# Performance work log

Hardware: AMD Instinct MI355X
Metric: run time of the kernel (lower is better)

Reference implementation:

```python
import jax, jax.numpy as jnp
import numpy as np

B, N, F_IN, OUT = 1, 8192, 256, 64

def setup_inputs() -> dict:
    key = jax.random.key(0)
    k1, k2, k3, k4 = jax.random.split(key, 4)
    seq = jax.random.normal(k1, (B, N, F_IN), dtype=jnp.float32)
    bias_mat = jnp.zeros((B, N, N), dtype=jnp.float32)  # 0 = fully connected; -1e9 entries mask edges
    W1 = jax.random.normal(k2, (F_IN, OUT), dtype=jnp.float32) * 0.05
    a1 = jax.random.normal(k3, (OUT, 1), dtype=jnp.float32) * 0.05
    b1 = jnp.zeros((1,), dtype=jnp.float32)
    a2 = jax.random.normal(k4, (OUT, 1), dtype=jnp.float32) * 0.05
    b2 = jnp.zeros((1,), dtype=jnp.float32)
    return {"seq": seq, "bias_mat": bias_mat, "W1": W1, "a1": a1, "b1": b1, "a2": a2, "b2": b2}

def reference(seq, bias_mat, W1, a1, b1, a2, b2):
    # Conv1D(kernel=1) == matmul over the feature dim
    seq_fts = jnp.einsum('bnf,fo->bno', seq, W1)          # [B,N,OUT]
    f_1 = jnp.einsum('bno,ok->bnk', seq_fts, a1) + b1      # [B,N,1]
    f_2 = jnp.einsum('bno,ok->bnk', seq_fts, a2) + b2      # [B,N,1]
    logits = f_1 + jnp.swapaxes(f_2, 1, 2)                  # [B,N,N] additive outer-sum
    coefs = jax.nn.softmax(jax.nn.leaky_relu(logits, negative_slope=0.2) + bias_mat, axis=-1)
    vals = jnp.einsum('bnm,bmo->bno', coefs, seq_fts)       # [B,N,OUT]
    return jax.nn.elu(vals)
```

## Files before the change

kernel.cpp:

```cpp
#include <hip/hip_runtime.h>
#include <hip/hip_bf16.h>


typedef float f32x4 __attribute__((ext_vector_type(4)));
typedef short bf16x8 __attribute__((ext_vector_type(8)));

__device__ __forceinline__ unsigned short f2bf(float x) {
    union { float f; unsigned u; } v; v.f = x;
    unsigned r = v.u + 0x7FFF + ((v.u >> 16) & 1);
    return (unsigned short)(r >> 16);
}

__device__ __forceinline__ float elu1(float x) {
    return x > 0.f ? x : (__expf(x) - 1.f);
}

__global__ __launch_bounds__(256) void attn_fts(
    const float* __restrict__ seq, const float* __restrict__ W1,
    const float* __restrict__ a1, const float* __restrict__ b1,
    const float* __restrict__ a2, const float* __restrict__ b2,
    unsigned short* __restrict__ ftsT, float* __restrict__ f1g,
    float* __restrict__ f2g)
{
    __shared__ unsigned short w1t[64 * 264];
    __shared__ unsigned short stage[64 * 40];
    __shared__ float f1p[2][32];
    __shared__ float f2p[2][32];

    const int tid = threadIdx.x;
    const int qb = blockIdx.x * 32;
    const int w = tid >> 6, rg = w & 1, oh = w >> 1;
    const int lane = tid & 63, c = lane & 15, g = lane >> 4;

    for (int i = 0; i < 64; ++i) {
        int e = tid + i * 256;
        int k = e >> 6, o = e & 63;
        w1t[o * 264 + k] = f2bf(W1[e]);
    }
    __syncthreads();

    f32x4 acc[2] = {};
    const float* srow = seq + (long)(qb + rg * 16 + c) * 256;
    #pragma unroll
    for (int ks = 0; ks < 8; ++ks) {
        int k0 = ks * 32 + g * 8;
        float4 s0 = *(const float4*)(srow + k0);
        float4 s1 = *(const float4*)(srow + k0 + 4);
        bf16x8 af;
        af[0] = (short)f2bf(s0.x); af[1] = (short)f2bf(s0.y);
        af[2] = (short)f2bf(s0.z); af[3] = (short)f2bf(s0.w);
        af[4] = (short)f2bf(s1.x); af[5] = (short)f2bf(s1.y);
        af[6] = (short)f2bf(s1.z); af[7] = (short)f2bf(s1.w);
        #pragma unroll
        for (int ob = 0; ob < 2; ++ob) {
            int brow = oh * 32 + ob * 16 + c;
            bf16x8 bf = *(const bf16x8*)(&w1t[brow * 264 + k0]);
            acc[ob] = __builtin_amdgcn_mfma_f32_16x16x32_bf16(af, bf, acc[ob], 0, 0, 0);
        }
    }

    float a1v0 = a1[oh * 32 + c], a1v1 = a1[oh * 32 + 16 + c];
    float a2v0 = a2[oh * 32 + c], a2v1 = a2[oh * 32 + 16 + c];
    #pragma unroll
    for (int reg = 0; reg < 4; ++reg) {
        float p1 = acc[0][reg] * a1v0 + acc[1][reg] * a1v1;
        float p2 = acc[0][reg] * a2v0 + acc[1][reg] * a2v1;
        #pragma unroll
        for (int mm = 1; mm < 16; mm <<= 1) {
            p1 += __shfl_xor(p1, mm, 64);
            p2 += __shfl_xor(p2, mm, 64);
        }
        if (c == 0) {
            f1p[oh][rg * 16 + g * 4 + reg] = p1;
            f2p[oh][rg * 16 + g * 4 + reg] = p2;
        }
    }

    #pragma unroll
    for (int ob = 0; ob < 2; ++ob) {
        int row = oh * 32 + ob * 16 + c;
        #pragma unroll
        for (int rp = 0; rp < 2; ++rp) {
            unsigned short lo = f2bf(acc[ob][rp * 2]);
            unsigned short hi = f2bf(acc[ob][rp * 2 + 1]);
            unsigned v = (unsigned)lo | ((unsigned)hi << 16);
            *(unsigned*)(&stage[row * 40 + rg * 16 + g * 4 + rp * 2]) = v;
        }
    }
    __syncthreads();

    {
        int o = tid >> 2, q4 = tid & 3;
        uint4 v = *(const uint4*)(&stage[o * 40 + q4 * 8]);
        *(uint4*)(&ftsT[(long)o * 8192 + qb + q4 * 8]) = v;
    }
    if (tid < 32) {
        f1g[qb + tid] = f1p[0][tid] + f1p[1][tid] + b1[0];
        f2g[qb + tid] = f2p[0][tid] + f2p[1][tid] + b2[0];
    }
}

__global__ __launch_bounds__(512) void attn_main(
    const float* __restrict__ bias, const unsigned short* __restrict__ ftsT,
    const float* __restrict__ f1g, const float* __restrict__ f2g,
    float* __restrict__ out)
{
    __shared__ float bias_lds[2][32][132];
    __shared__ unsigned short fts_lds[2][64][136];
    __shared__ float macc[2][4][16][68];
    __shared__ float mlm[2][4][16];
    __shared__ float mll[2][4][16];

    const int tid = threadIdx.x;
    const int qb = blockIdx.x * 32;
    const int w = tid >> 6, rg = w & 1, h = w >> 1;
    const int lane = tid & 63, c = lane & 15, g = lane >> 4;

    const int srow = tid >> 4;
    const int ssub = tid & 15;
    const long brow_base = (long)(qb + srow) * 8192;
    const int frow = tid >> 3;
    const int fchunk = tid & 7;

    const float f1r = f1g[qb + rg * 16 + c];

    float4 pb0, pb1, pf2a, pf2b;
    uint4 pf0, pf1;
    {
        const float* bp = bias + brow_base + ssub * 8;
        pb0 = ((const float4*)bp)[0];
        pb1 = ((const float4*)bp)[1];
        const unsigned short* fp = ftsT + (long)frow * 8192 + fchunk * 16;
        pf0 = ((const uint4*)fp)[0];
        pf1 = ((const uint4*)fp)[1];
        const float* f2p_ = f2g + h * 32 + g * 8;
        pf2a = ((const float4*)f2p_)[0];
        pf2b = ((const float4*)f2p_)[1];
    }

    float m = -INFINITY, lsum = 0.f;
    f32x4 acc[4] = {};

    for (int r = 0; r < 64; ++r) {
        const int buf = r & 1;
        __syncthreads();
        *(float4*)(&bias_lds[buf][srow][ssub * 8]) = pb0;
        *(float4*)(&bias_lds[buf][srow][ssub * 8 + 4]) = pb1;
        *(uint4*)(&fts_lds[buf][frow][fchunk * 16]) = pf0;
        *(uint4*)(&fts_lds[buf][frow][fchunk * 16 + 8]) = pf1;
        float f2v[8];
        f2v[0] = pf2a.x; f2v[1] = pf2a.y; f2v[2] = pf2a.z; f2v[3] = pf2a.w;
        f2v[4] = pf2b.x; f2v[5] = pf2b.y; f2v[6] = pf2b.z; f2v[7] = pf2b.w;
        if (r + 1 < 64) {
            const int j0 = (r + 1) * 128;
            const float* bp = bias + brow_base + j0 + ssub * 8;
            pb0 = ((const float4*)bp)[0];
            pb1 = ((const float4*)bp)[1];
            const unsigned short* fp = ftsT + (long)frow * 8192 + j0 + fchunk * 16;
            pf0 = ((const uint4*)fp)[0];
            pf1 = ((const uint4*)fp)[1];
            const float* f2p_ = f2g + j0 + h * 32 + g * 8;
            pf2a = ((const float4*)f2p_)[0];
            pf2b = ((const float4*)f2p_)[1];
        }
        __syncthreads();

        float4 s0 = *(const float4*)(&bias_lds[buf][rg * 16 + c][h * 32 + g * 8]);
        float4 s1 = *(const float4*)(&bias_lds[buf][rg * 16 + c][h * 32 + g * 8 + 4]);
        float bb[8] = { s0.x, s0.y, s0.z, s0.w, s1.x, s1.y, s1.z, s1.w };
        float s[8];
        float tm = -INFINITY;
        #pragma unroll
        for (int i = 0; i < 8; ++i) {
            float z = f1r + f2v[i];
            z = fmaxf(z, 0.2f * z);
            float sv = z + bb[i];
            s[i] = sv;
            tm = fmaxf(tm, sv);
        }
        tm = fmaxf(tm, __shfl_xor(tm, 16, 64));
        tm = fmaxf(tm, __shfl_xor(tm, 32, 64));
        const float mnew = fmaxf(m, tm);
        const float sc = __expf(m - mnew);
        float ts = 0.f;
        bf16x8 af;
        #pragma unroll
        for (int i = 0; i < 8; ++i) {
            float p = __expf(s[i] - mnew);
            ts += p;
            af[i] = (short)f2bf(p);
        }
        ts += __shfl_xor(ts, 16, 64);
        ts += __shfl_xor(ts, 32, 64);
        lsum = lsum * sc + ts;
        m = mnew;
        float scq[4];
        #pragma unroll
        for (int reg = 0; reg < 4; ++reg) scq[reg] = __shfl(sc, g * 4 + reg, 64);
        #pragma unroll
        for (int ob = 0; ob < 4; ++ob) {
            #pragma unroll
            for (int reg = 0; reg < 4; ++reg) acc[ob][reg] *= scq[reg];
        }
        #pragma unroll
        for (int ob = 0; ob < 4; ++ob) {
            bf16x8 bfrag = *(const bf16x8*)(&fts_lds[buf][ob * 16 + c][h * 32 + g * 8]);
            acc[ob] = __builtin_amdgcn_mfma_f32_16x16x32_bf16(af, bfrag, acc[ob], 0, 0, 0);
        }
    }

    __syncthreads();
    #pragma unroll
    for (int ob = 0; ob < 4; ++ob) {
        #pragma unroll
        for (int reg = 0; reg < 4; ++reg)
            macc[rg][h][g * 4 + reg][ob * 16 + c] = acc[ob][reg];
    }
    if (lane < 16) { mlm[rg][h][c] = m; mll[rg][h][c] = lsum; }
    __syncthreads();

    {
        const int row = tid >> 4;
        const int o0 = (tid & 15) * 4;
        const int rg2 = row >> 4, rr = row & 15;
        float m0 = mlm[rg2][0][rr], m1 = mlm[rg2][1][rr];
        float m2 = mlm[rg2][2][rr], m3 = mlm[rg2][3][rr];
        float ms = fmaxf(fmaxf(m0, m1), fmaxf(m2, m3));
        float w0 = __expf(m0 - ms), w1 = __expf(m1 - ms);
        float w2 = __expf(m2 - ms), w3 = __expf(m3 - ms);
        float den = mll[rg2][0][rr] * w0 + mll[rg2][1][rr] * w1 +
                    mll[rg2][2][rr] * w2 + mll[rg2][3][rr] * w3;
        float inv = 1.f / den;
        float4 v0 = *(const float4*)(&macc[rg2][0][rr][o0]);
        float4 v1 = *(const float4*)(&macc[rg2][1][rr][o0]);
        float4 v2 = *(const float4*)(&macc[rg2][2][rr][o0]);
        float4 v3 = *(const float4*)(&macc[rg2][3][rr][o0]);
        float4 res;
        res.x = elu1((v0.x * w0 + v1.x * w1 + v2.x * w2 + v3.x * w3) * inv);
        res.y = elu1((v0.y * w0 + v1.y * w1 + v2.y * w2 + v3.y * w3) * inv);
        res.z = elu1((v0.z * w0 + v1.z * w1 + v2.z * w2 + v3.z * w3) * inv);
        res.w = elu1((v0.w * w0 + v1.w * w1 + v2.w * w2 + v3.w * w3) * inv);
        *(float4*)(&out[(long)(qb + row) * 64 + o0]) = res;
    }
}

extern "C" void kernel_launch(void* const* d_in, const int* in_sizes, int n_in,
                              void* d_out, int out_size, void* d_ws, size_t ws_size,
                              hipStream_t stream) {
    (void)in_sizes; (void)n_in; (void)out_size; (void)ws_size;
    const float* seq  = (const float*)d_in[0];
    const float* bias = (const float*)d_in[1];
    const float* W1   = (const float*)d_in[2];
    const float* a1   = (const float*)d_in[3];
    const float* b1   = (const float*)d_in[4];
    const float* a2   = (const float*)d_in[5];
    const float* b2   = (const float*)d_in[6];
    float* out = (float*)d_out;

    unsigned short* ftsT = (unsigned short*)d_ws;
    float* f1 = (float*)((char*)d_ws + 64 * 8192 * 2);
    float* f2 = (float*)((char*)d_ws + 64 * 8192 * 2 + 8192 * 4);

    hipLaunchKernelGGL(attn_fts, dim3(256), dim3(256), 0, stream,
                       seq, W1, a1, b1, a2, b2, ftsT, f1, f2);
    hipLaunchKernelGGL(attn_main, dim3(256), dim3(512), 0, stream,
                       bias, ftsT, f1, f2, out);
}
```

Baseline: 385.6 us.

## Restructure attention main loop: 16-row blocks, direct fts loads, lazy rescale

Each block now handles 16 query rows instead of 32, so the grid grows from 256 to 512 blocks. Each of 8 waves takes a 32-column slice of a 256-wide key tile. The feature fragments are loaded straight from global memory into registers with A/B double buffering, which drops the LDS staging for fts; only the bias tile goes through LDS. The online softmax rescale is skipped unless the new max exceeds the running max by more than 8 (a lazy rescale). The end-of-block merge now combines 8 partial states per row. Doubling the blocks improves occupancy on 256 CUs, but each block reads ftsT independently from L2, so that traffic roughly doubles. The extra register buffers may also pressure occupancy.

```diff
diff --git a/kernel.cpp b/kernel.cpp
--- a/kernel.cpp
+++ b/kernel.cpp
@@ -100,74 +100,69 @@
     }
 }
 
-__global__ __launch_bounds__(512) void attn_main(
+__global__ __launch_bounds__(512, 4) void attn_main(
     const float* __restrict__ bias, const unsigned short* __restrict__ ftsT,
     const float* __restrict__ f1g, const float* __restrict__ f2g,
     float* __restrict__ out)
 {
-    __shared__ float bias_lds[2][32][132];
-    __shared__ unsigned short fts_lds[2][64][136];
-    __shared__ float macc[2][4][16][68];
-    __shared__ float mlm[2][4][16];
-    __shared__ float mll[2][4][16];
+    __shared__ float bias_lds[16][260];
+    __shared__ float macc[8][16][68];
+    __shared__ float mlm[8][16];
+    __shared__ float mll[8][16];
 
     const int tid = threadIdx.x;
-    const int qb = blockIdx.x * 32;
-    const int w = tid >> 6, rg = w & 1, h = w >> 1;
+    const int qb = blockIdx.x * 16;
+    const int h = tid >> 6;
     const int lane = tid & 63, c = lane & 15, g = lane >> 4;
 
-    const int srow = tid >> 4;
-    const int ssub = tid & 15;
-    const long brow_base = (long)(qb + srow) * 8192;
-    const int frow = tid >> 3;
-    const int fchunk = tid & 7;
-
-    const float f1r = f1g[qb + rg * 16 + c];
-
-    float4 pb0, pb1, pf2a, pf2b;
-    uint4 pf0, pf1;
-    {
-        const float* bp = bias + brow_base + ssub * 8;
-        pb0 = ((const float4*)bp)[0];
-        pb1 = ((const float4*)bp)[1];
-        const unsigned short* fp = ftsT + (long)frow * 8192 + fchunk * 16;
-        pf0 = ((const uint4*)fp)[0];
-        pf1 = ((const uint4*)fp)[1];
-        const float* f2p_ = f2g + h * 32 + g * 8;
-        pf2a = ((const float4*)f2p_)[0];
-        pf2b = ((const float4*)f2p_)[1];
-    }
+    const int srow = tid >> 5, schunk = tid & 31;
+    const float* bias_base = bias + (long)(qb + srow) * 8192 + schunk * 8;
+
+    const float f1r = f1g[qb + c];
+    const unsigned short* fts_base = ftsT + (long)c * 8192 + h * 32 + g * 8;
+    const float* f2_base = f2g + h * 32 + g * 8;
+
+    float4 bA0, bA1, bB0, bB1;
+    bf16x8 fA0, fA1, fA2, fA3, fB0, fB1, fB2, fB3;
+    float4 f2Aa, f2Ab, f2Ba, f2Bb;
+
+    auto issue_biasA = [&](int r) {
+        const float* p = bias_base + r * 256;
+        bA0 = ((const float4*)p)[0]; bA1 = ((const float4*)p)[1];
+    };
+    auto issue_biasB = [&](int r) {
+        const float* p = bias_base + r * 256;
+        bB0 = ((const float4*)p)[0]; bB1 = ((const float4*)p)[1];
+    };
+    auto issue_ftsA = [&](int r) {
+        const unsigned short* p = fts_base + r * 256;
+        fA0 = *(const bf16x8*)(p);
+        fA1 = *(const bf16x8*)(p + 16 * 8192);
+        fA2 = *(const bf16x8*)(p + 32 * 8192);
+        fA3 = *(const bf16x8*)(p + 48 * 8192);
+        const float* q = f2_base + r * 256;
+        f2Aa = ((const float4*)q)[0]; f2Ab = ((const float4*)q)[1];
+    };
+    auto issue_ftsB = [&](int r) {
+        const unsigned short* p = fts_base + r * 256;
+        fB0 = *(const bf16x8*)(p);
+        fB1 = *(const bf16x8*)(p + 16 * 8192);
+        fB2 = *(const bf16x8*)(p + 32 * 8192);
+        fB3 = *(const bf16x8*)(p + 48 * 8192);
+        const float* q = f2_base + r * 256;
+        f2Ba = ((const float4*)q)[0]; f2Bb = ((const float4*)q)[1];
+    };
 
     float m = -INFINITY, lsum = 0.f;
     f32x4 acc[4] = {};
 
-    for (int r = 0; r < 64; ++r) {
-        const int buf = r & 1;
-        __syncthreads();
-        *(float4*)(&bias_lds[buf][srow][ssub * 8]) = pb0;
-        *(float4*)(&bias_lds[buf][srow][ssub * 8 + 4]) = pb1;
-        *(uint4*)(&fts_lds[buf][frow][fchunk * 16]) = pf0;
-        *(uint4*)(&fts_lds[buf][frow][fchunk * 16 + 8]) = pf1;
-        float f2v[8];
-        f2v[0] = pf2a.x; f2v[1] = pf2a.y; f2v[2] = pf2a.z; f2v[3] = pf2a.w;
-        f2v[4] = pf2b.x; f2v[5] = pf2b.y; f2v[6] = pf2b.z; f2v[7] = pf2b.w;
-        if (r + 1 < 64) {
-            const int j0 = (r + 1) * 128;
-            const float* bp = bias + brow_base + j0 + ssub * 8;
-            pb0 = ((const float4*)bp)[0];
-            pb1 = ((const float4*)bp)[1];
-            const unsigned short* fp = ftsT + (long)frow * 8192 + j0 + fchunk * 16;
-            pf0 = ((const uint4*)fp)[0];
-            pf1 = ((const uint4*)fp)[1];
-            const float* f2p_ = f2g + j0 + h * 32 + g * 8;
-            pf2a = ((const float4*)f2p_)[0];
-            pf2b = ((const float4*)f2p_)[1];
-        }
-        __syncthreads();
-
-        float4 s0 = *(const float4*)(&bias_lds[buf][rg * 16 + c][h * 32 + g * 8]);
-        float4 s1 = *(const float4*)(&bias_lds[buf][rg * 16 + c][h * 32 + g * 8 + 4]);
-        float bb[8] = { s0.x, s0.y, s0.z, s0.w, s1.x, s1.y, s1.z, s1.w };
+    auto do_round = [&](const bf16x8& ff0, const bf16x8& ff1,
+                        const bf16x8& ff2, const bf16x8& ff3,
+                        const float4& fa, const float4& fb) {
+        float4 s0v = *(const float4*)(&bias_lds[c][h * 32 + g * 8]);
+        float4 s1v = *(const float4*)(&bias_lds[c][h * 32 + g * 8 + 4]);
+        float bb[8] = { s0v.x, s0v.y, s0v.z, s0v.w, s1v.x, s1v.y, s1v.z, s1v.w };
+        float f2v[8] = { fa.x, fa.y, fa.z, fa.w, fb.x, fb.y, fb.z, fb.w };
         float s[8];
         float tm = -INFINITY;
         #pragma unroll
@@ -180,66 +175,85 @@
         }
         tm = fmaxf(tm, __shfl_xor(tm, 16, 64));
         tm = fmaxf(tm, __shfl_xor(tm, 32, 64));
-        const float mnew = fmaxf(m, tm);
-        const float sc = __expf(m - mnew);
+        if (!__all(tm <= m + 8.f)) {
+            float mnew = fmaxf(m, tm);
+            float sc = __expf(m - mnew);
+            lsum *= sc;
+            float scq[4];
+            #pragma unroll
+            for (int reg = 0; reg < 4; ++reg) scq[reg] = __shfl(sc, g * 4 + reg, 64);
+            #pragma unroll
+            for (int ob = 0; ob < 4; ++ob)
+                #pragma unroll
+                for (int reg = 0; reg < 4; ++reg) acc[ob][reg] *= scq[reg];
+            m = mnew;
+        }
         float ts = 0.f;
         bf16x8 af;
         #pragma unroll
         for (int i = 0; i < 8; ++i) {
-            float p = __expf(s[i] - mnew);
+            float p = __expf(s[i] - m);
             ts += p;
             af[i] = (short)f2bf(p);
         }
         ts += __shfl_xor(ts, 16, 64);
         ts += __shfl_xor(ts, 32, 64);
-        lsum = lsum * sc + ts;
-        m = mnew;
-        float scq[4];
-        #pragma unroll
-        for (int reg = 0; reg < 4; ++reg) scq[reg] = __shfl(sc, g * 4 + reg, 64);
-        #pragma unroll
-        for (int ob = 0; ob < 4; ++ob) {
-            #pragma unroll
-            for (int reg = 0; reg < 4; ++reg) acc[ob][reg] *= scq[reg];
-        }
-        #pragma unroll
-        for (int ob = 0; ob < 4; ++ob) {
-            bf16x8 bfrag = *(const bf16x8*)(&fts_lds[buf][ob * 16 + c][h * 32 + g * 8]);
-            acc[ob] = __builtin_amdgcn_mfma_f32_16x16x32_bf16(af, bfrag, acc[ob], 0, 0, 0);
-        }
-    }
-
-    __syncthreads();
-    #pragma unroll
-    for (int ob = 0; ob < 4; ++ob) {
+        lsum += ts;
+        acc[0] = __builtin_amdgcn_mfma_f32_16x16x32_bf16(af, ff0, acc[0], 0, 0, 0);
+        acc[1] = __builtin_amdgcn_mfma_f32_16x16x32_bf16(af, ff1, acc[1], 0, 0, 0);
+        acc[2] = __builtin_amdgcn_mfma_f32_16x16x32_bf16(af, ff2, acc[2], 0, 0, 0);
+        acc[3] = __builtin_amdgcn_mfma_f32_16x16x32_bf16(af, ff3, acc[3], 0, 0, 0);
+    };
+
+    issue_biasA(0); issue_ftsA(0);
+    issue_biasB(1); issue_ftsB(1);
+
+    #pragma unroll 1
+    for (int rp = 0; rp < 16; ++rp) {
+        __syncthreads();
+        *(float4*)(&bias_lds[srow][schunk * 8]) = bA0;
+        *(float4*)(&bias_lds[srow][schunk * 8 + 4]) = bA1;
+        if (rp < 15) issue_biasA(2 * rp + 2);
+        __syncthreads();
+        do_round(fA0, fA1, fA2, fA3, f2Aa, f2Ab);
+        if (rp < 15) issue_ftsA(2 * rp + 2);
+        __syncthreads();
+        *(float4*)(&bias_lds[srow][schunk * 8]) = bB0;
+        *(float4*)(&bias_lds[srow][schunk * 8 + 4]) = bB1;
+        if (rp < 15) issue_biasB(2 * rp + 3);
+        __syncthreads();
+        do_round(fB0, fB1, fB2, fB3, f2Ba, f2Bb);
+        if (rp < 15) issue_ftsB(2 * rp + 3);
+    }
+
+    __syncthreads();
+    #pragma unroll
+    for (int ob = 0; ob < 4; ++ob)
         #pragma unroll
         for (int reg = 0; reg < 4; ++reg)
-            macc[rg][h][g * 4 + reg][ob * 16 + c] = acc[ob][reg];
-    }
-    if (lane < 16) { mlm[rg][h][c] = m; mll[rg][h][c] = lsum; }
-    __syncthreads();
-
-    {
+            macc[h][g * 4 + reg][ob * 16 + c] = acc[ob][reg];
+    if (lane < 16) { mlm[h][c] = m; mll[h][c] = lsum; }
+    __syncthreads();
+
+    if (tid < 256) {
         const int row = tid >> 4;
         const int o0 = (tid & 15) * 4;
-        const int rg2 = row >> 4, rr = row & 15;
-        float m0 = mlm[rg2][0][rr], m1 = mlm[rg2][1][rr];
-        float m2 = mlm[rg2][2][rr], m3 = mlm[rg2][3][rr];
-        float ms = fmaxf(fmaxf(m0, m1), fmaxf(m2, m3));
-        float w0 = __expf(m0 - ms), w1 = __expf(m1 - ms);
-        float w2 = __expf(m2 - ms), w3 = __expf(m3 - ms);
-        float den = mll[rg2][0][rr] * w0 + mll[rg2][1][rr] * w1 +
-                    mll[rg2][2][rr] * w2 + mll[rg2][3][rr] * w3;
+        float ms = -INFINITY;
+        #pragma unroll
+        for (int sI = 0; sI < 8; ++sI) ms = fmaxf(ms, mlm[sI][row]);
+        float den = 0.f;
+        float vx = 0.f, vy = 0.f, vz = 0.f, vw = 0.f;
+        #pragma unroll
+        for (int sI = 0; sI < 8; ++sI) {
+            float ws = __expf(mlm[sI][row] - ms);
+            den += mll[sI][row] * ws;
+            float4 a = *(const float4*)(&macc[sI][row][o0]);
+            vx += a.x * ws; vy += a.y * ws; vz += a.z * ws; vw += a.w * ws;
+        }
         float inv = 1.f / den;
-        float4 v0 = *(const float4*)(&macc[rg2][0][rr][o0]);
-        float4 v1 = *(const float4*)(&macc[rg2][1][rr][o0]);
-        float4 v2 = *(const float4*)(&macc[rg2][2][rr][o0]);
-        float4 v3 = *(const float4*)(&macc[rg2][3][rr][o0]);
         float4 res;
-        res.x = elu1((v0.x * w0 + v1.x * w1 + v2.x * w2 + v3.x * w3) * inv);
-        res.y = elu1((v0.y * w0 + v1.y * w1 + v2.y * w2 + v3.y * w3) * inv);
-        res.z = elu1((v0.z * w0 + v1.z * w1 + v2.z * w2 + v3.z * w3) * inv);
-        res.w = elu1((v0.w * w0 + v1.w * w1 + v2.w * w2 + v3.w * w3) * inv);
+        res.x = elu1(vx * inv); res.y = elu1(vy * inv);
+        res.z = elu1(vz * inv); res.w = elu1(vw * inv);
         *(float4*)(&out[(long)(qb + row) * 64 + o0]) = res;
     }
 }
@@ -263,6 +277,6 @@
 
     hipLaunchKernelGGL(attn_fts, dim3(256), dim3(256), 0, stream,
                        seq, W1, a1, b1, a2, b2, ftsT, f1, f2);
-    hipLaunchKernelGGL(attn_main, dim3(256), dim3(512), 0, stream,
+    hipLaunchKernelGGL(attn_main, dim3(512), dim3(512), 0, stream,
                        bias, ftsT, f1, f2, out);
 }
```

Result: no change. 386.8 us (+0.3%).

## Load fts fragments directly to registers, widen bias tiles, add lazy max rescaling

Applied to the files above, without the earlier changes.

The main attention kernel no longer stages the bf16 feature matrix through LDS. Each wave loads its MFMA B-fragments straight from global memory into double-buffered registers (A/B sets), interleaved with compute. The bias tile grows from 128 to 512 columns per sync, cutting barriers from 64 to 16 iterations. The online softmax now only rescales the accumulators when the new max exceeds the running max by more than 8, which skips most rescale multiplies and shuffles. The costs are redundant global reads of fts across the row-group waves, more registers, and reliance on exp(s-m) staying bounded within the threshold.

```diff
diff --git a/kernel.cpp b/kernel.cpp
--- a/kernel.cpp
+++ b/kernel.cpp
@@ -105,8 +105,7 @@
     const float* __restrict__ f1g, const float* __restrict__ f2g,
     float* __restrict__ out)
 {
-    __shared__ float bias_lds[2][32][132];
-    __shared__ unsigned short fts_lds[2][64][136];
+    __shared__ float blds[32][516];
     __shared__ float macc[2][4][16][68];
     __shared__ float mlm[2][4][16];
     __shared__ float mll[2][4][16];
@@ -116,58 +115,54 @@
     const int w = tid >> 6, rg = w & 1, h = w >> 1;
     const int lane = tid & 63, c = lane & 15, g = lane >> 4;
 
-    const int srow = tid >> 4;
-    const int ssub = tid & 15;
-    const long brow_base = (long)(qb + srow) * 8192;
-    const int frow = tid >> 3;
-    const int fchunk = tid & 7;
+    const int srow = tid >> 4, schunk = tid & 15;
+    const float* bias_base = bias + (long)(qb + srow) * 8192 + schunk * 8;
 
     const float f1r = f1g[qb + rg * 16 + c];
-
-    float4 pb0, pb1, pf2a, pf2b;
-    uint4 pf0, pf1;
-    {
-        const float* bp = bias + brow_base + ssub * 8;
-        pb0 = ((const float4*)bp)[0];
-        pb1 = ((const float4*)bp)[1];
-        const unsigned short* fp = ftsT + (long)frow * 8192 + fchunk * 16;
-        pf0 = ((const uint4*)fp)[0];
-        pf1 = ((const uint4*)fp)[1];
-        const float* f2p_ = f2g + h * 32 + g * 8;
-        pf2a = ((const float4*)f2p_)[0];
-        pf2b = ((const float4*)f2p_)[1];
-    }
+    const unsigned short* fts_base = ftsT + (long)c * 8192 + h * 128 + g * 8;
+    const float* f2_base = f2g + h * 128 + g * 8;
+
+    float4 pb[8];
+    auto issue_bias = [&](int r) {
+        const float* p = bias_base + r * 512;
+        #pragma unroll
+        for (int k = 0; k < 4; ++k) {
+            pb[2 * k]     = ((const float4*)(p + k * 128))[0];
+            pb[2 * k + 1] = ((const float4*)(p + k * 128))[1];
+        }
+    };
+
+    bf16x8 fA[4], fB[4];
+    float4 f2A0, f2A1, f2B0, f2B1;
+    auto issue_ftsA = [&](int r, int ks) {
+        const unsigned short* p = fts_base + r * 512 + ks * 32;
+        fA[0] = *(const bf16x8*)(p);
+        fA[1] = *(const bf16x8*)(p + 16 * 8192);
+        fA[2] = *(const bf16x8*)(p + 32 * 8192);
+        fA[3] = *(const bf16x8*)(p + 48 * 8192);
+        const float* q = f2_base + r * 512 + ks * 32;
+        f2A0 = ((const float4*)q)[0]; f2A1 = ((const float4*)q)[1];
+    };
+    auto issue_ftsB = [&](int r, int ks) {
+        const unsigned short* p = fts_base + r * 512 + ks * 32;
+        fB[0] = *(const bf16x8*)(p);
+        fB[1] = *(const bf16x8*)(p + 16 * 8192);
+        fB[2] = *(const bf16x8*)(p + 32 * 8192);
+        fB[3] = *(const bf16x8*)(p + 48 * 8192);
+        const float* q = f2_base + r * 512 + ks * 32;
+        f2B0 = ((const float4*)q)[0]; f2B1 = ((const float4*)q)[1];
+    };
 
     float m = -INFINITY, lsum = 0.f;
     f32x4 acc[4] = {};
 
-    for (int r = 0; r < 64; ++r) {
-        const int buf = r & 1;
-        __syncthreads();
-        *(float4*)(&bias_lds[buf][srow][ssub * 8]) = pb0;
-        *(float4*)(&bias_lds[buf][srow][ssub * 8 + 4]) = pb1;
-        *(uint4*)(&fts_lds[buf][frow][fchunk * 16]) = pf0;
-        *(uint4*)(&fts_lds[buf][frow][fchunk * 16 + 8]) = pf1;
-        float f2v[8];
-        f2v[0] = pf2a.x; f2v[1] = pf2a.y; f2v[2] = pf2a.z; f2v[3] = pf2a.w;
-        f2v[4] = pf2b.x; f2v[5] = pf2b.y; f2v[6] = pf2b.z; f2v[7] = pf2b.w;
-        if (r + 1 < 64) {
-            const int j0 = (r + 1) * 128;
-            const float* bp = bias + brow_base + j0 + ssub * 8;
-            pb0 = ((const float4*)bp)[0];
-            pb1 = ((const float4*)bp)[1];
-            const unsigned short* fp = ftsT + (long)frow * 8192 + j0 + fchunk * 16;
-            pf0 = ((const uint4*)fp)[0];
-            pf1 = ((const uint4*)fp)[1];
-            const float* f2p_ = f2g + j0 + h * 32 + g * 8;
-            pf2a = ((const float4*)f2p_)[0];
-            pf2b = ((const float4*)f2p_)[1];
-        }
-        __syncthreads();
-
-        float4 s0 = *(const float4*)(&bias_lds[buf][rg * 16 + c][h * 32 + g * 8]);
-        float4 s1 = *(const float4*)(&bias_lds[buf][rg * 16 + c][h * 32 + g * 8 + 4]);
-        float bb[8] = { s0.x, s0.y, s0.z, s0.w, s1.x, s1.y, s1.z, s1.w };
+    auto do_ks = [&](int jcol, const bf16x8 (&ff)[4],
+                     const float4& fa, const float4& fb) {
+        const float* bl = &blds[rg * 16 + c][jcol];
+        float4 b0 = *(const float4*)(bl);
+        float4 b1v = *(const float4*)(bl + 4);
+        float bb[8] = { b0.x, b0.y, b0.z, b0.w, b1v.x, b1v.y, b1v.z, b1v.w };
+        float f2v[8] = { fa.x, fa.y, fa.z, fa.w, fb.x, fb.y, fb.z, fb.w };
         float s[8];
         float tm = -INFINITY;
         #pragma unroll
@@ -180,42 +175,68 @@
         }
         tm = fmaxf(tm, __shfl_xor(tm, 16, 64));
         tm = fmaxf(tm, __shfl_xor(tm, 32, 64));
-        const float mnew = fmaxf(m, tm);
-        const float sc = __expf(m - mnew);
+        if (!__all(tm <= m + 8.f)) {
+            float mnew = fmaxf(m, tm);
+            float sc = __expf(m - mnew);
+            lsum *= sc;
+            float scq[4];
+            #pragma unroll
+            for (int reg = 0; reg < 4; ++reg) scq[reg] = __shfl(sc, g * 4 + reg, 64);
+            #pragma unroll
+            for (int ob = 0; ob < 4; ++ob)
+                #pragma unroll
+                for (int reg = 0; reg < 4; ++reg) acc[ob][reg] *= scq[reg];
+            m = mnew;
+        }
         float ts = 0.f;
         bf16x8 af;
         #pragma unroll
         for (int i = 0; i < 8; ++i) {
-            float p = __expf(s[i] - mnew);
+            float p = __expf(s[i] - m);
             ts += p;
             af[i] = (short)f2bf(p);
         }
         ts += __shfl_xor(ts, 16, 64);
         ts += __shfl_xor(ts, 32, 64);
-        lsum = lsum * sc + ts;
-        m = mnew;
-        float scq[4];
-        #pragma unroll
-        for (int reg = 0; reg < 4; ++reg) scq[reg] = __shfl(sc, g * 4 + reg, 64);
-        #pragma unroll
-        for (int ob = 0; ob < 4; ++ob) {
-            #pragma unroll
-            for (int reg = 0; reg < 4; ++reg) acc[ob][reg] *= scq[reg];
-        }
-        #pragma unroll
-        for (int ob = 0; ob < 4; ++ob) {
-            bf16x8 bfrag = *(const bf16x8*)(&fts_lds[buf][ob * 16 + c][h * 32 + g * 8]);
-            acc[ob] = __builtin_amdgcn_mfma_f32_16x16x32_bf16(af, bfrag, acc[ob], 0, 0, 0);
-        }
-    }
-
-    __syncthreads();
-    #pragma unroll
-    for (int ob = 0; ob < 4; ++ob) {
+        lsum += ts;
+        acc[0] = __builtin_amdgcn_mfma_f32_16x16x32_bf16(af, ff[0], acc[0], 0, 0, 0);
+        acc[1] = __builtin_amdgcn_mfma_f32_16x16x32_bf16(af, ff[1], acc[1], 0, 0, 0);
+        acc[2] = __builtin_amdgcn_mfma_f32_16x16x32_bf16(af, ff[2], acc[2], 0, 0, 0);
+        acc[3] = __builtin_amdgcn_mfma_f32_16x16x32_bf16(af, ff[3], acc[3], 0, 0, 0);
+    };
+
+    const int jc0 = h * 128 + g * 8;
+
+    issue_bias(0);
+    issue_ftsA(0, 0);
+
+    #pragma unroll 1
+    for (int r = 0; r < 16; ++r) {
+        __syncthreads();
+        #pragma unroll
+        for (int k = 0; k < 4; ++k) {
+            *(float4*)(&blds[srow][k * 128 + schunk * 8])     = pb[2 * k];
+            *(float4*)(&blds[srow][k * 128 + schunk * 8 + 4]) = pb[2 * k + 1];
+        }
+        if (r < 15) issue_bias(r + 1);
+        __syncthreads();
+
+        issue_ftsB(r, 1);
+        do_ks(jc0,      fA, f2A0, f2A1);
+        issue_ftsA(r, 2);
+        do_ks(jc0 + 32, fB, f2B0, f2B1);
+        issue_ftsB(r, 3);
+        do_ks(jc0 + 64, fA, f2A0, f2A1);
+        if (r < 15) issue_ftsA(r + 1, 0);
+        do_ks(jc0 + 96, fB, f2B0, f2B1);
+    }
+
+    __syncthreads();
+    #pragma unroll
+    for (int ob = 0; ob < 4; ++ob)
         #pragma unroll
         for (int reg = 0; reg < 4; ++reg)
             macc[rg][h][g * 4 + reg][ob * 16 + c] = acc[ob][reg];
-    }
     if (lane < 16) { mlm[rg][h][c] = m; mll[rg][h][c] = lsum; }
     __syncthreads();
 
```

Measured after the change: 459.1 us. 1.19x slower.
